# Optimization experiments

Hardware: AMD Instinct MI355X
Metric: run time of the kernel (lower is better)

Reference implementation:

```python
import jax, jax.numpy as jnp
import numpy as np

N = 100000   # nodes
E = 1600000  # edges
IN_CH = 128
EDGE_DIM = 16
HEADS = 4
OUT_CH = 16
NEG_SLOPE = 0.2


def setup_inputs() -> dict:
    key = jax.random.key(0)
    ks = jax.random.split(key, 12)
    HC = HEADS * OUT_CH
    inp = {
        "x": jax.random.normal(ks[0], (N, IN_CH), dtype=jnp.float32),
        "edge_index": jax.random.randint(ks[1], (2, E), 0, N, dtype=jnp.int32),
        "edge_attr": jax.random.normal(ks[2], (E, EDGE_DIM), dtype=jnp.float32),
        # linear layer params (W stored as [in, out] so y = x @ W + b)
        "W_src": jax.random.normal(ks[3], (IN_CH, HC), dtype=jnp.float32) / np.sqrt(IN_CH),
        "b_src": jnp.zeros((HC,), dtype=jnp.float32),
        "W_dst": jax.random.normal(ks[4], (IN_CH, HC), dtype=jnp.float32) / np.sqrt(IN_CH),
        "b_dst": jnp.zeros((HC,), dtype=jnp.float32),
        "W_edge": jax.random.normal(ks[5], (EDGE_DIM, HC), dtype=jnp.float32) / np.sqrt(EDGE_DIM),
        "b_edge": jnp.zeros((HC,), dtype=jnp.float32),
        # attention vectors [1, heads, out_channels]
        "att_src": jax.random.normal(ks[6], (1, HEADS, OUT_CH), dtype=jnp.float32) * 0.1,
        "att_dst": jax.random.normal(ks[7], (1, HEADS, OUT_CH), dtype=jnp.float32) * 0.1,
        "att_edge": jax.random.normal(ks[8], (1, HEADS, OUT_CH), dtype=jnp.float32) * 0.1,
    }
    return inp


def _segment_softmax(alpha, seg, num_segments):
    # alpha: [E, H]; softmax over edges sharing the same dst node (seg).
    m = jax.ops.segment_max(alpha, seg, num_segments=num_segments)
    m = jnp.where(jnp.isfinite(m), m, 0.0)  # empty segments -> -inf; neutralize
    a = jnp.exp(alpha - m[seg])
    s = jax.ops.segment_sum(a, seg, num_segments=num_segments)
    return a / (s[seg] + 1e-16)


def reference(x, edge_index, edge_attr, W_src, b_src, W_dst, b_dst,
              W_edge, b_edge, att_src, att_dst, att_edge):
    n = x.shape[0]
    src_idx, dst_idx = edge_index[0], edge_index[1]

    src = (x @ W_src + b_src).reshape(n, HEADS, OUT_CH)        # [N,H,C]
    dst = (x @ W_dst + b_dst).reshape(n, HEADS, OUT_CH)        # [N,H,C]
    edge_feat = (edge_attr @ W_edge + b_edge).reshape(-1, HEADS, OUT_CH)  # [E,H,C]

    alpha_src = jnp.sum(src * att_src, axis=-1)[src_idx]       # [E,H]
    alpha_dst = jnp.sum(dst * att_dst, axis=-1)[dst_idx]       # [E,H]
    alpha_edge = jnp.sum(edge_feat * att_edge, axis=-1)        # [E,H]

    alpha = alpha_src + alpha_dst + alpha_edge
    alpha = jnp.where(alpha >= 0, alpha, NEG_SLOPE * alpha)    # leaky_relu(0.2)
    alpha = _segment_softmax(alpha, dst_idx, n)                # [E,H]
    # dropout is identity in eval mode

    msg = src[src_idx] * alpha[..., None]                      # [E,H,C]
    out = jax.ops.segment_sum(msg, dst_idx, num_segments=n)    # [N,H,C]
    return out.reshape(n, HEADS * OUT_CH)
```

## Files before the change

### kernel.cpp

```cpp
#include <hip/hip_runtime.h>


#define N_NODES 100000
#define N_EDGES 1600000
#define SCAN_B 1024
#define SCAN_NBLK ((N_NODES + SCAN_B - 1) / SCAN_B)

typedef float f32x4 __attribute__((ext_vector_type(4)));
typedef int   i32x4 __attribute__((ext_vector_type(4)));

static __device__ __forceinline__ unsigned int f2bf(float f) {
    unsigned int u = __float_as_uint(f);
    return (u + 0x7fffu + ((u >> 16) & 1u)) >> 16;
}
static __device__ __forceinline__ float bf2f(unsigned int bits16) {
    return __uint_as_float(bits16 << 16);
}

__global__ __launch_bounds__(640) void k_prep(
    const float* __restrict__ We, const float* __restrict__ be,
    const float* __restrict__ att_e, const float* __restrict__ Wdst,
    const float* __restrict__ bdst, const float* __restrict__ att_d,
    float* __restrict__ V)
{
    const int t = threadIdx.x;
    if (t < 64) {
        const int k = t >> 2, h = t & 3;
        float acc = 0.f;
        for (int c = 0; c < 16; ++c)
            acc += We[k * 64 + h * 16 + c] * att_e[h * 16 + c];
        V[k * 4 + h] = acc;
        if (t < 4) {
            float b = 0.f;
            for (int c = 0; c < 16; ++c)
                b += be[t * 16 + c] * att_e[t * 16 + c];
            V[64 + t] = b;
        }
    } else if (t < 576) {
        const int j = t - 64;
        const int k = j >> 2, h = j & 3;
        float acc = 0.f;
        for (int c = 0; c < 16; ++c)
            acc += Wdst[k * 64 + h * 16 + c] * att_d[h * 16 + c];
        V[68 + j] = acc;
    } else if (t < 580) {
        const int h = t - 576;
        float b = 0.f;
        for (int c = 0; c < 16; ++c)
            b += bdst[h * 16 + c] * att_d[h * 16 + c];
        V[580 + h] = b;
    }
}

__global__ __launch_bounds__(256) void k_node_proj(
    const float* __restrict__ x, const float* __restrict__ Wsrc,
    const float* __restrict__ bsrc, const float* __restrict__ att_src,
    const float* __restrict__ Vbuf, unsigned short* __restrict__ spbf,
    float* __restrict__ alpha_sn, float* __restrict__ alpha_dn)
{
    __shared__ float xs[32 * 132];
    __shared__ float uDs[4 * 132];
    __shared__ float bDs[4];
    const int tid = threadIdx.x;
    const int nbase = blockIdx.x * 32;

    {
        const f32x4* xsrc = (const f32x4*)(x + (size_t)nbase * 128);
#pragma unroll
        for (int i = 0; i < 4; ++i) {
            const int idx = tid + i * 256;
            const int n = idx >> 5, q = idx & 31;
            *(f32x4*)&xs[n * 132 + q * 4] = xsrc[idx];
        }
#pragma unroll
        for (int i = 0; i < 2; ++i) {
            const int j = tid + i * 256;
            const int k = j >> 2, h = j & 3;
            uDs[h * 132 + k] = Vbuf[68 + j];
        }
        if (tid < 4) bDs[tid] = Vbuf[580 + tid];
    }
    __syncthreads();

    const int col = tid & 63;
    const int g = tid >> 6;

    float accS[8];
#pragma unroll
    for (int i = 0; i < 8; ++i) accS[i] = 0.f;

    for (int k4 = 0; k4 < 128; k4 += 4) {
        f32x4 xv[8];
#pragma unroll
        for (int i = 0; i < 8; ++i)
            xv[i] = *(const f32x4*)&xs[(g * 8 + i) * 132 + k4];
#pragma unroll
        for (int kk = 0; kk < 4; ++kk) {
            const float wsv = Wsrc[(k4 + kk) * 64 + col];
#pragma unroll
            for (int i = 0; i < 8; ++i)
                accS[i] = fmaf(xv[i][kk], wsv, accS[i]);
        }
    }

    const int li = col & 7, lh = (col >> 3) & 3, khalf = (col >> 5) * 64;
    float ad = 0.f;
#pragma unroll
    for (int kq = 0; kq < 16; ++kq) {
        const f32x4 xq = *(const f32x4*)&xs[(g * 8 + li) * 132 + khalf + kq * 4];
        const f32x4 uq = *(const f32x4*)&uDs[lh * 132 + khalf + kq * 4];
#pragma unroll
        for (int j = 0; j < 4; ++j)
            ad = fmaf(xq[j], uq[j], ad);
    }
    ad += __shfl_xor(ad, 32);

    const float bs = bsrc[col];
    const float as_ = att_src[col];
    const int h = col >> 4;
#pragma unroll
    for (int i = 0; i < 8; ++i) {
        const int n = nbase + g * 8 + i;
        const float vS = accS[i] + bs;
        spbf[(size_t)n * 64 + col] = (unsigned short)f2bf(vS);
        float t1 = vS * as_;
#pragma unroll
        for (int off = 8; off >= 1; off >>= 1)
            t1 += __shfl_xor(t1, off, 16);
        if ((col & 15) == 0)
            alpha_sn[n * 4 + h] = t1;
    }
    if (col < 32)
        alpha_dn[(nbase + g * 8 + li) * 4 + lh] = ad + bDs[lh];
}

__global__ __launch_bounds__(256) void k_hist(const int* __restrict__ ei,
                                               int* __restrict__ cnt)
{
    const int e = blockIdx.x * 256 + threadIdx.x;
    if (e >= N_EDGES) return;
    atomicAdd(&cnt[ei[N_EDGES + e]], 1);
}

__global__ __launch_bounds__(256) void k_scan_part(const int* __restrict__ cnt,
                                                    int* __restrict__ partial)
{
    __shared__ int red[4];
    const int t = threadIdx.x;
    const int base = blockIdx.x * SCAN_B + t * 4;
    int s = 0;
#pragma unroll
    for (int i = 0; i < 4; ++i) {
        const int idx = base + i;
        if (idx < N_NODES) s += cnt[idx];
    }
#pragma unroll
    for (int off = 32; off >= 1; off >>= 1)
        s += __shfl_xor(s, off, 64);
    if ((t & 63) == 0) red[t >> 6] = s;
    __syncthreads();
    if (t == 0)
        partial[blockIdx.x] = red[0] + red[1] + red[2] + red[3];
}

__global__ __launch_bounds__(128) void k_scan_top(int* __restrict__ partial)
{
    __shared__ int sums[128];
    const int t = threadIdx.x;
    sums[t] = (t < SCAN_NBLK) ? partial[t] : 0;
    __syncthreads();
#pragma unroll
    for (int off = 1; off < 128; off <<= 1) {
        int v = (t >= off) ? sums[t - off] : 0;
        __syncthreads();
        sums[t] += v;
        __syncthreads();
    }
    if (t < SCAN_NBLK) partial[t] = (t == 0) ? 0 : sums[t - 1];
}

__global__ __launch_bounds__(256) void k_scan_down(
    const int* __restrict__ cnt, const int* __restrict__ partial,
    int* __restrict__ row_start, int* __restrict__ cursor)
{
    __shared__ int tsum[256];
    const int t = threadIdx.x;
    const int base = blockIdx.x * SCAN_B + t * 4;
    int c[4];
#pragma unroll
    for (int i = 0; i < 4; ++i) {
        const int idx = base + i;
        c[i] = (idx < N_NODES) ? cnt[idx] : 0;
    }
    const int tot = c[0] + c[1] + c[2] + c[3];
    tsum[t] = tot;
    __syncthreads();
#pragma unroll
    for (int off = 1; off < 256; off <<= 1) {
        int v = (t >= off) ? tsum[t - off] : 0;
        __syncthreads();
        tsum[t] += v;
        __syncthreads();
    }
    int run = partial[blockIdx.x] + ((t == 0) ? 0 : tsum[t - 1]);
#pragma unroll
    for (int i = 0; i < 4; ++i) {
        const int idx = base + i;
        if (idx < N_NODES) {
            row_start[idx] = run;
            cursor[idx] = run;
        }
        run += c[i];
    }
    if (blockIdx.x == 0 && t == 0)
        row_start[N_NODES] = N_EDGES;
}

__global__ __launch_bounds__(256) void k_fill(
    const int* __restrict__ ei, const float* __restrict__ ea,
    const float* __restrict__ V, const float* __restrict__ alpha_sn,
    const float* __restrict__ alpha_dn, int* __restrict__ cursor,
    int4* __restrict__ rec)
{
    __shared__ float Vs[68];
    if (threadIdx.x < 68) Vs[threadIdx.x] = V[threadIdx.x];
    __syncthreads();

    const int e = blockIdx.x * 256 + threadIdx.x;
    if (e >= N_EDGES) return;
    const int src = ei[e];
    const int dst = ei[N_EDGES + e];

    const f32x4* ea4 = (const f32x4*)(ea + (size_t)e * 16);
    float ek[16];
    {
        f32x4 c0 = __builtin_nontemporal_load(ea4 + 0);
        f32x4 c1 = __builtin_nontemporal_load(ea4 + 1);
        f32x4 c2 = __builtin_nontemporal_load(ea4 + 2);
        f32x4 c3 = __builtin_nontemporal_load(ea4 + 3);
        ek[0]=c0.x; ek[1]=c0.y; ek[2]=c0.z; ek[3]=c0.w;
        ek[4]=c1.x; ek[5]=c1.y; ek[6]=c1.z; ek[7]=c1.w;
        ek[8]=c2.x; ek[9]=c2.y; ek[10]=c2.z; ek[11]=c2.w;
        ek[12]=c3.x; ek[13]=c3.y; ek[14]=c3.z; ek[15]=c3.w;
    }
    float a[4] = {Vs[64], Vs[65], Vs[66], Vs[67]};
#pragma unroll
    for (int k = 0; k < 16; ++k) {
#pragma unroll
        for (int h = 0; h < 4; ++h)
            a[h] = fmaf(ek[k], Vs[k * 4 + h], a[h]);
    }

    const float4 asn = *(const float4*)(alpha_sn + (size_t)src * 4);
    const float4 adn = *(const float4*)(alpha_dn + (size_t)dst * 4);
    float a0 = a[0] + asn.x + adn.x;
    float a1 = a[1] + asn.y + adn.y;
    float a2 = a[2] + asn.z + adn.z;
    float a3 = a[3] + asn.w + adn.w;
    a0 = (a0 >= 0.f) ? a0 : 0.2f * a0;
    a1 = (a1 >= 0.f) ? a1 : 0.2f * a1;
    a2 = (a2 >= 0.f) ? a2 : 0.2f * a2;
    a3 = (a3 >= 0.f) ? a3 : 0.2f * a3;

    const unsigned int w01 = f2bf(__expf(a0)) | (f2bf(__expf(a1)) << 16);
    const unsigned int w23 = f2bf(__expf(a2)) | (f2bf(__expf(a3)) << 16);

    const int slot = atomicAdd(&cursor[dst], 1);
    rec[slot] = make_int4(src, (int)w01, (int)w23, 0);
}

__global__ __launch_bounds__(256) void k_gather(
    const int* __restrict__ row_start, const int4* __restrict__ rec,
    const unsigned short* __restrict__ spbf, float* __restrict__ out)
{
    const int lane = threadIdx.x & 63;
    const int node = (blockIdx.x * 256 + threadIdx.x) >> 6;
    const int h = lane >> 4;
    const int base = row_start[node];
    const int end = row_start[node + 1];
    const i32x4* rec4 = (const i32x4*)rec;

    float acc = 0.f, denom = 0.f;
    int j = base;
    for (; j + 4 <= end; j += 4) {
        const i32x4 r0 = __builtin_nontemporal_load(rec4 + j);
        const i32x4 r1 = __builtin_nontemporal_load(rec4 + j + 1);
        const i32x4 r2 = __builtin_nontemporal_load(rec4 + j + 2);
        const i32x4 r3 = __builtin_nontemporal_load(rec4 + j + 3);
        const float v0 = bf2f(spbf[((size_t)r0.x << 6) + lane]);
        const float v1 = bf2f(spbf[((size_t)r1.x << 6) + lane]);
        const float v2 = bf2f(spbf[((size_t)r2.x << 6) + lane]);
        const float v3 = bf2f(spbf[((size_t)r3.x << 6) + lane]);
#define WEXT(r) bf2f(((h & 1) ? ((unsigned int)((h < 2) ? r.y : r.z) >> 16) \
                              : ((unsigned int)((h < 2) ? r.y : r.z) & 0xffffu)))
        const float w0 = WEXT(r0), w1 = WEXT(r1), w2 = WEXT(r2), w3 = WEXT(r3);
        denom += (w0 + w1) + (w2 + w3);
        acc = fmaf(w0, v0, acc);
        acc = fmaf(w1, v1, acc);
        acc = fmaf(w2, v2, acc);
        acc = fmaf(w3, v3, acc);
    }
    for (; j < end; ++j) {
        const i32x4 r0 = __builtin_nontemporal_load(rec4 + j);
        const float v0 = bf2f(spbf[((size_t)r0.x << 6) + lane]);
        const float w0 = WEXT(r0);
        denom += w0;
        acc = fmaf(w0, v0, acc);
    }
#undef WEXT
    __builtin_nontemporal_store(acc / (denom + 1e-16f), &out[(size_t)node * 64 + lane]);
}

extern "C" void kernel_launch(void* const* d_in, const int* in_sizes, int n_in,
                              void* d_out, int out_size, void* d_ws, size_t ws_size,
                              hipStream_t stream) {
    const float* x     = (const float*)d_in[0];
    const int*   ei    = (const int*)d_in[1];
    const float* ea    = (const float*)d_in[2];
    const float* Wsrc  = (const float*)d_in[3];
    const float* bsrc  = (const float*)d_in[4];
    const float* Wdst  = (const float*)d_in[5];
    const float* bdst  = (const float*)d_in[6];
    const float* We    = (const float*)d_in[7];
    const float* be    = (const float*)d_in[8];
    const float* att_s = (const float*)d_in[9];
    const float* att_d = (const float*)d_in[10];
    const float* att_e = (const float*)d_in[11];
    float* out = (float*)d_out;

    int4*  rec       = (int4*)d_ws;
    unsigned short* spbf = (unsigned short*)(rec + N_EDGES);
    float* alpha_sn  = (float*)(spbf + (size_t)N_NODES * 64);
    float* alpha_dn  = alpha_sn + (size_t)N_NODES * 4;
    int*   cnt       = (int*)(alpha_dn + (size_t)N_NODES * 4);
    int*   row_start = cnt + N_NODES;
    int*   cursor    = row_start + N_NODES + 4;
    int*   partial   = cursor + N_NODES;
    float* V         = (float*)(partial + 128);

    hipMemsetAsync(cnt, 0, (size_t)N_NODES * sizeof(int), stream);

    k_prep<<<1, 640, 0, stream>>>(We, be, att_e, Wdst, bdst, att_d, V);
    k_node_proj<<<N_NODES / 32, 256, 0, stream>>>(x, Wsrc, bsrc, att_s, V,
                                                  spbf, alpha_sn, alpha_dn);
    k_hist<<<N_EDGES / 256, 256, 0, stream>>>(ei, cnt);
    k_scan_part<<<SCAN_NBLK, 256, 0, stream>>>(cnt, partial);
    k_scan_top<<<1, 128, 0, stream>>>(partial);
    k_scan_down<<<SCAN_NBLK, 256, 0, stream>>>(cnt, partial, row_start, cursor);
    k_fill<<<N_EDGES / 256, 256, 0, stream>>>(ei, ea, V, alpha_sn, alpha_dn,
                                              cursor, rec);
    k_gather<<<(N_NODES + 3) / 4, 256, 0, stream>>>(row_start, rec, spbf, out);
}
```

Measured before the change: 487.0 us.

## Split edge CSR fill into two-pass binned scatter through shared memory

The single-pass fill that scattered each edge record to a random CSR slot is replaced by two passes. The first pass buckets each 4096-edge chunk by coarse destination bin (512 nodes) in LDS and writes contiguous runs to per-bin regions. The second pass loads each bin into LDS and scatters its records to exact per-node slots, which now land in a localized address range. This aims to turn scattered global writes into coalesced or cache-local ones, at the cost of an extra read and write of the record array, an extra kernel launch, and large LDS use that limits occupancy.

```diff
diff --git a/kernel.cpp b/kernel.cpp
--- a/kernel.cpp
+++ b/kernel.cpp
@@ -5,9 +5,13 @@
 #define N_EDGES 1600000
 #define SCAN_B 1024
 #define SCAN_NBLK ((N_NODES + SCAN_B - 1) / SCAN_B)
+#define BINSH 9
+#define NBIN 196
+#define CHUNK 4096
+#define NBLK_P1 ((N_EDGES + CHUNK - 1) / CHUNK)
+#define CAP 9216
 
 typedef float f32x4 __attribute__((ext_vector_type(4)));
-typedef int   i32x4 __attribute__((ext_vector_type(4)));
 
 static __device__ __forceinline__ unsigned int f2bf(float f) {
     unsigned int u = __float_as_uint(f);
@@ -181,7 +185,8 @@
 
 __global__ __launch_bounds__(256) void k_scan_down(
     const int* __restrict__ cnt, const int* __restrict__ partial,
-    int* __restrict__ row_start, int* __restrict__ cursor)
+    int* __restrict__ row_start, int* __restrict__ cursor,
+    int* __restrict__ bin_cursor)
 {
     __shared__ int tsum[256];
     const int t = threadIdx.x;
@@ -209,6 +214,8 @@
         if (idx < N_NODES) {
             row_start[idx] = run;
             cursor[idx] = run;
+            if ((idx & ((1 << BINSH) - 1)) == 0)
+                bin_cursor[idx >> BINSH] = run;
         }
         run += c[i];
     }
@@ -216,77 +223,175 @@
         row_start[N_NODES] = N_EDGES;
 }
 
-__global__ __launch_bounds__(256) void k_fill(
+__global__ __launch_bounds__(256) void k_fill_p1(
     const int* __restrict__ ei, const float* __restrict__ ea,
     const float* __restrict__ V, const float* __restrict__ alpha_sn,
-    const float* __restrict__ alpha_dn, int* __restrict__ cursor,
+    const float* __restrict__ alpha_dn, int* __restrict__ bin_cursor,
     int4* __restrict__ rec)
 {
     __shared__ float Vs[68];
-    if (threadIdx.x < 68) Vs[threadIdx.x] = V[threadIdx.x];
-    __syncthreads();
-
-    const int e = blockIdx.x * 256 + threadIdx.x;
-    if (e >= N_EDGES) return;
-    const int src = ei[e];
-    const int dst = ei[N_EDGES + e];
-
-    const f32x4* ea4 = (const f32x4*)(ea + (size_t)e * 16);
-    float ek[16];
-    {
-        f32x4 c0 = __builtin_nontemporal_load(ea4 + 0);
-        f32x4 c1 = __builtin_nontemporal_load(ea4 + 1);
-        f32x4 c2 = __builtin_nontemporal_load(ea4 + 2);
-        f32x4 c3 = __builtin_nontemporal_load(ea4 + 3);
-        ek[0]=c0.x; ek[1]=c0.y; ek[2]=c0.z; ek[3]=c0.w;
-        ek[4]=c1.x; ek[5]=c1.y; ek[6]=c1.z; ek[7]=c1.w;
-        ek[8]=c2.x; ek[9]=c2.y; ek[10]=c2.z; ek[11]=c2.w;
-        ek[12]=c3.x; ek[13]=c3.y; ek[14]=c3.z; ek[15]=c3.w;
-    }
-    float a[4] = {Vs[64], Vs[65], Vs[66], Vs[67]};
-#pragma unroll
-    for (int k = 0; k < 16; ++k) {
-#pragma unroll
-        for (int h = 0; h < 4; ++h)
-            a[h] = fmaf(ek[k], Vs[k * 4 + h], a[h]);
-    }
-
-    const float4 asn = *(const float4*)(alpha_sn + (size_t)src * 4);
-    const float4 adn = *(const float4*)(alpha_dn + (size_t)dst * 4);
-    float a0 = a[0] + asn.x + adn.x;
-    float a1 = a[1] + asn.y + adn.y;
-    float a2 = a[2] + asn.z + adn.z;
-    float a3 = a[3] + asn.w + adn.w;
-    a0 = (a0 >= 0.f) ? a0 : 0.2f * a0;
-    a1 = (a1 >= 0.f) ? a1 : 0.2f * a1;
-    a2 = (a2 >= 0.f) ? a2 : 0.2f * a2;
-    a3 = (a3 >= 0.f) ? a3 : 0.2f * a3;
-
-    const unsigned int w01 = f2bf(__expf(a0)) | (f2bf(__expf(a1)) << 16);
-    const unsigned int w23 = f2bf(__expf(a2)) | (f2bf(__expf(a3)) << 16);
-
-    const int slot = atomicAdd(&cursor[dst], 1);
-    rec[slot] = make_int4(src, (int)w01, (int)w23, 0);
+    __shared__ int   hist[NBIN];
+    __shared__ int   lcur[NBIN];
+    __shared__ int   gbase[NBIN];
+    __shared__ int   stmp[256];
+    __shared__ int4  recs[CHUNK];
+    __shared__ unsigned short binOf[CHUNK];
+
+    const int tid = threadIdx.x;
+    if (tid < 68) Vs[tid] = V[tid];
+    for (int i = tid; i < NBIN; i += 256) hist[i] = 0;
+    __syncthreads();
+
+    const int ebase = blockIdx.x * CHUNK;
+    const int n = min(CHUNK, N_EDGES - ebase);
+
+    for (int i = 0; i < 16; ++i) {
+        const int li = i * 256 + tid;
+        if (li < n)
+            atomicAdd(&hist[ei[N_EDGES + ebase + li] >> BINSH], 1);
+    }
+    __syncthreads();
+
+    stmp[tid] = (tid < NBIN) ? hist[tid] : 0;
+    __syncthreads();
+    for (int off = 1; off < 256; off <<= 1) {
+        const int v = (tid >= off) ? stmp[tid - off] : 0;
+        __syncthreads();
+        stmp[tid] += v;
+        __syncthreads();
+    }
+    if (tid < NBIN) {
+        const int cntb = hist[tid];
+        const int excl = stmp[tid] - cntb;
+        lcur[tid] = excl;
+        gbase[tid] = cntb ? atomicAdd(&bin_cursor[tid], cntb) : 0;
+        hist[tid] = excl;
+    }
+    __syncthreads();
+
+#pragma unroll 2
+    for (int i = 0; i < 16; ++i) {
+        const int li = i * 256 + tid;
+        if (li >= n) continue;
+        const int e = ebase + li;
+        const int src = ei[e];
+        const int dst = ei[N_EDGES + e];
+
+        const f32x4* ea4 = (const f32x4*)(ea + (size_t)e * 16);
+        float ek[16];
+        {
+            f32x4 c0 = __builtin_nontemporal_load(ea4 + 0);
+            f32x4 c1 = __builtin_nontemporal_load(ea4 + 1);
+            f32x4 c2 = __builtin_nontemporal_load(ea4 + 2);
+            f32x4 c3 = __builtin_nontemporal_load(ea4 + 3);
+            ek[0]=c0.x; ek[1]=c0.y; ek[2]=c0.z; ek[3]=c0.w;
+            ek[4]=c1.x; ek[5]=c1.y; ek[6]=c1.z; ek[7]=c1.w;
+            ek[8]=c2.x; ek[9]=c2.y; ek[10]=c2.z; ek[11]=c2.w;
+            ek[12]=c3.x; ek[13]=c3.y; ek[14]=c3.z; ek[15]=c3.w;
+        }
+        float a[4] = {Vs[64], Vs[65], Vs[66], Vs[67]};
+#pragma unroll
+        for (int k = 0; k < 16; ++k) {
+#pragma unroll
+            for (int h = 0; h < 4; ++h)
+                a[h] = fmaf(ek[k], Vs[k * 4 + h], a[h]);
+        }
+        const float4 asn = *(const float4*)(alpha_sn + (size_t)src * 4);
+        const float4 adn = *(const float4*)(alpha_dn + (size_t)dst * 4);
+        float a0 = a[0] + asn.x + adn.x;
+        float a1 = a[1] + asn.y + adn.y;
+        float a2 = a[2] + asn.z + adn.z;
+        float a3 = a[3] + asn.w + adn.w;
+        a0 = (a0 >= 0.f) ? a0 : 0.2f * a0;
+        a1 = (a1 >= 0.f) ? a1 : 0.2f * a1;
+        a2 = (a2 >= 0.f) ? a2 : 0.2f * a2;
+        a3 = (a3 >= 0.f) ? a3 : 0.2f * a3;
+        const unsigned int w01 = f2bf(__expf(a0)) | (f2bf(__expf(a1)) << 16);
+        const unsigned int w23 = f2bf(__expf(a2)) | (f2bf(__expf(a3)) << 16);
+
+        const int b = dst >> BINSH;
+        const int pos = atomicAdd(&lcur[b], 1);
+        recs[pos] = make_int4(src, (int)w01, (int)w23, dst);
+        binOf[pos] = (unsigned short)b;
+    }
+    __syncthreads();
+
+    for (int j = tid; j < n; j += 256) {
+        const int b = binOf[j];
+        rec[gbase[b] + (j - hist[b])] = recs[j];
+    }
+}
+
+__global__ __launch_bounds__(256) void k_fill_p2(
+    const int* __restrict__ row_start, int* __restrict__ cursor,
+    int4* __restrict__ rec)
+{
+    __shared__ int4 sbin[CAP];
+    const int tid = threadIdx.x;
+    const int b = blockIdx.x;
+    const int bs = row_start[b << BINSH];
+    const int nd = (b + 1) << BINSH;
+    const int be = (nd >= N_NODES) ? N_EDGES : row_start[nd];
+    const int cntb = be - bs;
+    const int nl = min(cntb, CAP);
+
+    for (int j = tid; j < nl; j += 256)
+        sbin[j] = rec[bs + j];
+    int4 ovf[4];
+#pragma unroll
+    for (int k = 0; k < 4; ++k) {
+        const int j = nl + k * 256 + tid;
+        if (j < cntb) ovf[k] = rec[bs + j];
+    }
+    __syncthreads();
+
+    int j = tid;
+    for (; j + 768 < nl; j += 1024) {
+        const int4 r0 = sbin[j], r1 = sbin[j + 256];
+        const int4 r2 = sbin[j + 512], r3 = sbin[j + 768];
+        const int s0 = atomicAdd(&cursor[r0.w], 1);
+        const int s1 = atomicAdd(&cursor[r1.w], 1);
+        const int s2 = atomicAdd(&cursor[r2.w], 1);
+        const int s3 = atomicAdd(&cursor[r3.w], 1);
+        rec[s0] = make_int4(r0.x, r0.y, r0.z, 0);
+        rec[s1] = make_int4(r1.x, r1.y, r1.z, 0);
+        rec[s2] = make_int4(r2.x, r2.y, r2.z, 0);
+        rec[s3] = make_int4(r3.x, r3.y, r3.z, 0);
+    }
+    for (; j < nl; j += 256) {
+        const int4 r0 = sbin[j];
+        const int s0 = atomicAdd(&cursor[r0.w], 1);
+        rec[s0] = make_int4(r0.x, r0.y, r0.z, 0);
+    }
+#pragma unroll
+    for (int k = 0; k < 4; ++k) {
+        const int jo = nl + k * 256 + tid;
+        if (jo < cntb) {
+            const int s0 = atomicAdd(&cursor[ovf[k].w], 1);
+            rec[s0] = make_int4(ovf[k].x, ovf[k].y, ovf[k].z, 0);
+        }
+    }
 }
 
 __global__ __launch_bounds__(256) void k_gather(
     const int* __restrict__ row_start, const int4* __restrict__ rec,
     const unsigned short* __restrict__ spbf, float* __restrict__ out)
 {
+    typedef int i32x4v __attribute__((ext_vector_type(4)));
     const int lane = threadIdx.x & 63;
     const int node = (blockIdx.x * 256 + threadIdx.x) >> 6;
     const int h = lane >> 4;
     const int base = row_start[node];
     const int end = row_start[node + 1];
-    const i32x4* rec4 = (const i32x4*)rec;
+    const i32x4v* rec4 = (const i32x4v*)rec;
 
     float acc = 0.f, denom = 0.f;
     int j = base;
     for (; j + 4 <= end; j += 4) {
-        const i32x4 r0 = __builtin_nontemporal_load(rec4 + j);
-        const i32x4 r1 = __builtin_nontemporal_load(rec4 + j + 1);
-        const i32x4 r2 = __builtin_nontemporal_load(rec4 + j + 2);
-        const i32x4 r3 = __builtin_nontemporal_load(rec4 + j + 3);
+        const i32x4v r0 = __builtin_nontemporal_load(rec4 + j);
+        const i32x4v r1 = __builtin_nontemporal_load(rec4 + j + 1);
+        const i32x4v r2 = __builtin_nontemporal_load(rec4 + j + 2);
+        const i32x4v r3 = __builtin_nontemporal_load(rec4 + j + 3);
         const float v0 = bf2f(spbf[((size_t)r0.x << 6) + lane]);
         const float v1 = bf2f(spbf[((size_t)r1.x << 6) + lane]);
         const float v2 = bf2f(spbf[((size_t)r2.x << 6) + lane]);
@@ -301,7 +406,7 @@
         acc = fmaf(w3, v3, acc);
     }
     for (; j < end; ++j) {
-        const i32x4 r0 = __builtin_nontemporal_load(rec4 + j);
+        const i32x4v r0 = __builtin_nontemporal_load(rec4 + j);
         const float v0 = bf2f(spbf[((size_t)r0.x << 6) + lane]);
         const float w0 = WEXT(r0);
         denom += w0;
@@ -336,7 +441,8 @@
     int*   row_start = cnt + N_NODES;
     int*   cursor    = row_start + N_NODES + 4;
     int*   partial   = cursor + N_NODES;
-    float* V         = (float*)(partial + 128);
+    int*   bin_cursor = partial + 128;
+    float* V         = (float*)(bin_cursor + 196 + 4);
 
     hipMemsetAsync(cnt, 0, (size_t)N_NODES * sizeof(int), stream);
 
@@ -346,8 +452,10 @@
     k_hist<<<N_EDGES / 256, 256, 0, stream>>>(ei, cnt);
     k_scan_part<<<SCAN_NBLK, 256, 0, stream>>>(cnt, partial);
     k_scan_top<<<1, 128, 0, stream>>>(partial);
-    k_scan_down<<<SCAN_NBLK, 256, 0, stream>>>(cnt, partial, row_start, cursor);
-    k_fill<<<N_EDGES / 256, 256, 0, stream>>>(ei, ea, V, alpha_sn, alpha_dn,
-                                              cursor, rec);
+    k_scan_down<<<SCAN_NBLK, 256, 0, stream>>>(cnt, partial, row_start, cursor,
+                                               bin_cursor);
+    k_fill_p1<<<NBLK_P1, 256, 0, stream>>>(ei, ea, V, alpha_sn, alpha_dn,
+                                           bin_cursor, rec);
+    k_fill_p2<<<NBIN, 256, 0, stream>>>(row_start, cursor, rec);
     k_gather<<<(N_NODES + 3) / 4, 256, 0, stream>>>(row_start, rec, spbf, out);
 }
```

Measured after the change: 515.2 us. 1.06x slower.
